# Kernel optimization log

Hardware: AMD Instinct MI355X
Metric: run time of the kernel (lower is better)

## Reference

```python
import jax, jax.numpy as jnp
import numpy as np

N = 100000
E = 1600000
F_IN = 256   # 4 * 64 after concat
H = 128

def _glorot(key, shape):
    fan_in, fan_out = shape
    lim = jnp.sqrt(6.0 / (fan_in + fan_out))
    return jax.random.uniform(key, shape, jnp.float32, -lim, lim)

def setup_inputs() -> dict:
    key = jax.random.key(0)
    ks = jax.random.split(key, 32)
    inp = {
        'x': jax.random.normal(ks[0], (N, 64), jnp.float32),
        'diff': jax.random.normal(ks[1], (N, 64), jnp.float32),
        'rec_prev': jax.random.normal(ks[2], (N, 64), jnp.float32),
        'hidden_prev': jax.random.normal(ks[3], (N, 64), jnp.float32),
        'edge_index': jax.random.randint(ks[4], (2, E), 0, N, jnp.int64),
    }
    dims = [(F_IN, H), (H, H), (H, H), (H, 1)]
    for i, (din, dout) in enumerate(dims):
        inp[f'Wl{i}'] = _glorot(ks[5 + 3 * i], (din, dout))  # neighbor (aggr) weight
        inp[f'Wr{i}'] = _glorot(ks[6 + 3 * i], (din, dout))  # root weight
        inp[f'b{i}'] = jnp.zeros((dout,), jnp.float32)
    return inp

def _sage_conv(h, src, dst, Wl, Wr, b):
    # mean aggregation of source-node features at destination nodes (PyG SAGEConv)
    msg_sum = jax.ops.segment_sum(h[src], dst, num_segments=N)        # [N, F]
    cnt = jax.ops.segment_sum(jnp.ones((src.shape[0],), h.dtype), dst, num_segments=N)
    mean = msg_sum / jnp.maximum(cnt, 1.0)[:, None]
    return mean @ Wl + h @ Wr + b

def reference(x, diff, rec_prev, hidden_prev, edge_index,
              Wl0, Wr0, b0, Wl1, Wr1, b1, Wl2, Wr2, b2, Wl3, Wr3, b3):
    src, dst = edge_index[0], edge_index[1]
    h = jnp.concatenate([x, diff, rec_prev, hidden_prev], axis=1)  # [N, 256]
    params = [(Wl0, Wr0, b0), (Wl1, Wr1, b1), (Wl2, Wr2, b2), (Wl3, Wr3, b3)]
    h = _sage_conv(h, src, dst, *params[0])
    for Wl, Wr, b in params[1:]:
        h = jax.nn.relu(h)
        h = _sage_conv(h, src, dst, Wl, Wr, b)
    out = jax.nn.sigmoid(h)          # [N, 1]
    lwp_util = jnp.mean(out)
    return out, lwp_util
```

## Files before the change

### kernel.cpp

```cpp
#include <hip/hip_runtime.h>
#include <hip/hip_bf16.h>

#define NN 100000
#define EE 1600000
#define HH 128
#define NB 391
#define CAP 5120
#define GB 1563

typedef short bf16x8 __attribute__((ext_vector_type(8)));
typedef short bf16x4 __attribute__((ext_vector_type(4)));
typedef float f32x4  __attribute__((ext_vector_type(4)));

__device__ inline short f2bf(float v) {
    __hip_bfloat16 b = __float2bfloat16(v);
    return *reinterpret_cast<short*>(&b);
}

typedef __attribute__((address_space(1))) void gvoid_t;
typedef __attribute__((address_space(3))) void svoid_t;
__device__ __forceinline__ void gload16(const void* g, void* l) {
    __builtin_amdgcn_global_load_lds((gvoid_t*)g, (svoid_t*)l, 16, 0, 0);
}

__device__ __forceinline__ void waitbar(int n) {
    if (n == 0)      asm volatile("s_waitcnt vmcnt(0)\n\ts_barrier" ::: "memory");
    else if (n == 2) asm volatile("s_waitcnt vmcnt(2)\n\ts_barrier" ::: "memory");
    else             asm volatile("s_waitcnt vmcnt(4)\n\ts_barrier" ::: "memory");
}

__global__ __launch_bounds__(1024) void prep_kernel(
    const float* __restrict__ Wl0, const float* __restrict__ Wr0,
    const float* __restrict__ Wl1, const float* __restrict__ Wr1,
    const float* __restrict__ Wl2, const float* __restrict__ Wr2,
    __hip_bfloat16* __restrict__ WT0, __hip_bfloat16* __restrict__ WT1,
    __hip_bfloat16* __restrict__ WT2, int* __restrict__ bcur) {
    const int t = threadIdx.x;
    if (blockIdx.x == 128) {
        if (t < NB) bcur[t] = 0;
        return;
    }
    int id = blockIdx.x * 1024 + t;
    if (id < 65536) {
        int k = id & 255, n = id >> 8;
        float v = (n < 128) ? Wl0[(size_t)k * 128 + n]
                            : Wr0[(size_t)k * 128 + (n - 128)];
        WT0[(size_t)n * 256 + k] = __float2bfloat16(v);
    } else {
        id -= 65536;
        int layer = id >> 15;
        int u = id & 32767;
        int k = u & 127, n = u >> 7;
        const float* Wl = layer ? Wl2 : Wl1;
        const float* Wr = layer ? Wr2 : Wr1;
        __hip_bfloat16* WT = layer ? WT2 : WT1;
        float v = (n < 128) ? Wl[(size_t)k * 128 + n]
                            : Wr[(size_t)k * 128 + (n - 128)];
        WT[(size_t)n * 128 + k] = __float2bfloat16(v);
    }
}

#define TSW 152
template <int K, bool FIRST>
__device__ __forceinline__ void gemm_body(
    short* __restrict__ lsh, int bid,
    const __hip_bfloat16* hin,
    const float* __restrict__ x0, const float* __restrict__ x1,
    const float* __restrict__ x2, const float* __restrict__ x3,
    const __hip_bfloat16* __restrict__ wt, const float* __restrict__ bias,
    __hip_bfloat16* zout, __hip_bfloat16* __restrict__ rout) {
    const int t    = threadIdx.x;
    const int w    = t >> 6;
    const int lane = t & 63;
    const int quad = lane >> 4;
    const int l16  = lane & 15;
    const int n0   = bid * 64;

    constexpr int NS   = K / 64;
    constexpr int BUFB = FIRST ? 16384 : 8192;
    constexpr int GPW  = FIRST ? 4 : 2;
    char* const lc = (char*)lsh;

    const __hip_bfloat16* afeat[4];
#pragma unroll
    for (int ft = 0; ft < 4; ++ft)
        afeat[ft] = wt + (size_t)(w * 64 + ft * 16 + l16) * K + quad * 8;

    f32x4 acc[4][4];
#pragma unroll
    for (int ft = 0; ft < 4; ++ft)
#pragma unroll
        for (int nt = 0; nt < 4; ++nt)
            acc[ft][nt] = (f32x4){0.f, 0.f, 0.f, 0.f};

    auto stage = [&](int p, int bb) {
        char* lb = lc + bb * BUFB;
        if constexpr (FIRST) {
            const float* sp = (p == 0) ? x0 : (p == 1) ? x1 : (p == 2) ? x2 : x3;
#pragma unroll
            for (int i = 0; i < 4; ++i) {
                const int j   = w * 4 + i;
                const int row = j * 4 + (lane >> 4);
                int rg = n0 + row; if (rg > NN - 1) rg = NN - 1;
                const int colb = ((lane & 15) * 16) ^ ((row & 15) << 4);
                gload16((const char*)sp + (size_t)rg * 256 + colb, lb + j * 1024);
            }
        } else {
#pragma unroll
            for (int i = 0; i < 2; ++i) {
                const int j   = w * 2 + i;
                const int row = j * 8 + (lane >> 3);
                int rg = n0 + row; if (rg > NN - 1) rg = NN - 1;
                const int colb = ((lane & 7) * 16) ^ ((row & 7) << 4);
                gload16((const char*)hin + (size_t)rg * 256 + p * 128 + colb,
                        lb + j * 1024);
            }
        }
    };

    auto compute = [&](int s) {
        const char* lb = lc + (s & 1) * BUFB;
#pragma unroll
        for (int kcl = 0; kcl < 2; ++kcl) {
            const int kc = s * 2 + kcl;
            bf16x8 af[4];
#pragma unroll
            for (int ft = 0; ft < 4; ++ft)
                af[ft] = *(const bf16x8*)(afeat[ft] + kc * 32);
#pragma unroll
            for (int nt = 0; nt < 4; ++nt) {
                const int row = nt * 16 + l16;
                bf16x8 b;
                if constexpr (FIRST) {
                    const int sw = (row & 15) << 4;
                    const int B0 = kcl * 128 + quad * 32;
                    const char* rb = lb + row * 256;
                    const f32x4 lo = *(const f32x4*)(rb + ((B0) ^ sw));
                    const f32x4 hi = *(const f32x4*)(rb + ((B0 + 16) ^ sw));
                    b[0] = f2bf(lo[0]); b[1] = f2bf(lo[1]);
                    b[2] = f2bf(lo[2]); b[3] = f2bf(lo[3]);
                    b[4] = f2bf(hi[0]); b[5] = f2bf(hi[1]);
                    b[6] = f2bf(hi[2]); b[7] = f2bf(hi[3]);
                } else {
                    const int sw = (row & 7) << 4;
                    const int B0 = kcl * 64 + quad * 16;
                    b = *(const bf16x8*)(lb + row * 128 + (B0 ^ sw));
                }
#pragma unroll
                for (int ft = 0; ft < 4; ++ft)
                    acc[ft][nt] = __builtin_amdgcn_mfma_f32_16x16x32_bf16(
                        af[ft], b, acc[ft][nt], 0, 0, 0);
            }
        }
    };

    stage(0, 0);
    stage(1, 1);
#pragma unroll
    for (int s = 0; s < NS; ++s) {
        waitbar(s < NS - 1 ? GPW : 0);
        compute(s);
        asm volatile("s_barrier" ::: "memory");
        if (s + 2 < NS) stage(s + 2, s & 1);
    }

    if (w < 2) {
#pragma unroll
        for (int ft = 0; ft < 4; ++ft) {
            const int fb = ft * 16 + quad * 4;
#pragma unroll
            for (int nt = 0; nt < 4; ++nt) {
                const f32x4 a = acc[ft][nt];
                bf16x4 p;
                p[0] = f2bf(a[0]); p[1] = f2bf(a[1]);
                p[2] = f2bf(a[2]); p[3] = f2bf(a[3]);
                *(bf16x4*)&lsh[(nt * 16 + l16) * TSW + w * 64 + fb] = p;
            }
        }
    }
    __syncthreads();
#pragma unroll
    for (int u = 0; u < 4; ++u) {
        const int id  = u * 256 + t;
        const int row = id >> 4, ch = (id & 15) * 8;
        const int nd  = n0 + row;
        if (nd < NN)
            *(bf16x8*)&zout[(size_t)nd * HH + ch] = *(const bf16x8*)&lsh[row * TSW + ch];
    }
    __syncthreads();

    if (w >= 2) {
        const int fcol = (w - 2) * 64;
#pragma unroll
        for (int ft = 0; ft < 4; ++ft) {
            const int fb = ft * 16 + quad * 4;
            const float4 bv = *(const float4*)&bias[fcol + fb];
#pragma unroll
            for (int nt = 0; nt < 4; ++nt) {
                const f32x4 a = acc[ft][nt];
                bf16x4 p;
                p[0] = f2bf(a[0] + bv.x); p[1] = f2bf(a[1] + bv.y);
                p[2] = f2bf(a[2] + bv.z); p[3] = f2bf(a[3] + bv.w);
                *(bf16x4*)&lsh[(nt * 16 + l16) * TSW + fcol + fb] = p;
            }
        }
    }
    __syncthreads();
#pragma unroll
    for (int u = 0; u < 4; ++u) {
        const int id  = u * 256 + t;
        const int row = id >> 4, ch = (id & 15) * 8;
        const int nd  = n0 + row;
        if (nd < NN)
            *(bf16x8*)&rout[(size_t)nd * HH + ch] = *(const bf16x8*)&lsh[row * TSW + ch];
    }
}

template <int K, bool FIRST>
__global__ __launch_bounds__(256) void gemm_kernel(
    const __hip_bfloat16* hin,
    const float* __restrict__ x0, const float* __restrict__ x1,
    const float* __restrict__ x2, const float* __restrict__ x3,
    const __hip_bfloat16* __restrict__ wt, const float* __restrict__ bias,
    __hip_bfloat16* zout, __hip_bfloat16* __restrict__ rout) {
    __shared__ short lsh[9728];
    gemm_body<K, FIRST>(lsh, blockIdx.x, hin, x0, x1, x2, x3, wt, bias, zout, rout);
}

__global__ __launch_bounds__(256) void gemm0_scatter_kernel(
    const float* __restrict__ x0, const float* __restrict__ x1,
    const float* __restrict__ x2, const float* __restrict__ x3,
    const __hip_bfloat16* __restrict__ wt, const float* __restrict__ bias,
    __hip_bfloat16* __restrict__ zout, __hip_bfloat16* __restrict__ rout,
    const int* __restrict__ srcv, const int* __restrict__ dstv,
    int* __restrict__ bcur, int* __restrict__ pairs) {
    __shared__ short lsh[16384];
    const int t = threadIdx.x;

    if (blockIdx.x >= NB) {
        gemm_body<256, true>(lsh, blockIdx.x - NB, nullptr, x0, x1, x2, x3,
                             wt, bias, zout, rout);
        return;
    }

    int* hist = (int*)lsh;
    int* base = hist + NB;
    for (int j = t; j < NB; j += 256) hist[j] = 0;
    __syncthreads();

    const int e0 = blockIdx.x * 4096;
    int s[16], d[16];
#pragma unroll
    for (int u = 0; u < 16; ++u) {
        const int e = e0 + u * 256 + t;
        if (e < EE) {
            s[u] = srcv[e]; d[u] = dstv[e];
            atomicAdd(&hist[d[u] >> 8], 1);
        } else {
            d[u] = -1;
        }
    }
    __syncthreads();

    for (int j = t; j < NB; j += 256)
        base[j] = hist[j] ? atomicAdd(&bcur[j], hist[j]) : 0;
    __syncthreads();
    for (int j = t; j < NB; j += 256) hist[j] = base[j];
    __syncthreads();

#pragma unroll
    for (int u = 0; u < 16; ++u)
        if (d[u] >= 0) {
            const int b   = d[u] >> 8;
            const int pos = atomicAdd(&hist[b], 1);
            if (pos < CAP) pairs[b * CAP + pos] = (s[u] << 8) | (d[u] & 255);
        }
}

__global__ __launch_bounds__(256) void finalize_kernel(
    const int* __restrict__ bcur, const int* __restrict__ pairs,
    int* __restrict__ csr, int* __restrict__ beg, int* __restrict__ eend,
    float* __restrict__ inv) {
    __shared__ int cnt[256];
    __shared__ int scn[256];
    __shared__ int cur[256];
    const int b = blockIdx.x, t = threadIdx.x;
    int m = bcur[b];
    if (m > CAP) m = CAP;

    cnt[t] = 0;
    __syncthreads();
    for (int e = t; e < m; e += 256)
        atomicAdd(&cnt[pairs[b * CAP + e] & 255], 1);
    __syncthreads();

    const int v = cnt[t];
    scn[t] = v;
    __syncthreads();
    for (int st = 1; st < 256; st <<= 1) {
        int tv = (t >= st) ? scn[t - st] : 0;
        __syncthreads();
        scn[t] += tv;
        __syncthreads();
    }
    const int myStart = scn[t] - v;
    cur[t] = myStart;
    __syncthreads();

    for (int e = t; e < m; e += 256) {
        const int pk  = pairs[b * CAP + e];
        const int pos = atomicAdd(&cur[pk & 255], 1);
        csr[b * CAP + pos] = pk >> 8;
    }

    const int node = b * 256 + t;
    if (node < NN) {
        beg[node]  = b * CAP + myStart;
        eend[node] = b * CAP + myStart + v;
        inv[node]  = 1.0f / fmaxf((float)v, 1.0f);
    }
}

template <bool LAST>
__global__ __launch_bounds__(256) void aggregate_kernel(
    const __hip_bfloat16* __restrict__ z, __hip_bfloat16* __restrict__ rio,
    const int* __restrict__ beg, const int* __restrict__ eend,
    const int* __restrict__ csr, const float* __restrict__ inv,
    const float* __restrict__ Wl3, const float* __restrict__ Wr3,
    const float* __restrict__ b3, float* __restrict__ z3,
    float* __restrict__ r3) {
    const int i    = (blockIdx.x * 256 + threadIdx.x) >> 6;
    const int lane = threadIdx.x & 63;
    const int g    = lane >> 4;
    const int l16  = lane & 15;
    if (i >= NN) return;
    const int b0 = beg[i], e0 = eend[i];

    float acc[8];
#pragma unroll
    for (int j = 0; j < 8; ++j) acc[j] = 0.f;

    int e = b0 + g;
    for (; e + 12 < e0; e += 16) {
        const int s0 = csr[e];
        const int s1 = csr[e + 4];
        const int s2 = csr[e + 8];
        const int s3 = csr[e + 12];
        const bf16x8 z0 = *(const bf16x8*)&z[(size_t)s0 * HH + l16 * 8];
        const bf16x8 z1 = *(const bf16x8*)&z[(size_t)s1 * HH + l16 * 8];
        const bf16x8 z2 = *(const bf16x8*)&z[(size_t)s2 * HH + l16 * 8];
        const bf16x8 z3v = *(const bf16x8*)&z[(size_t)s3 * HH + l16 * 8];
        const __hip_bfloat162* p0 = (const __hip_bfloat162*)&z0;
        const __hip_bfloat162* p1 = (const __hip_bfloat162*)&z1;
        const __hip_bfloat162* p2 = (const __hip_bfloat162*)&z2;
        const __hip_bfloat162* p3 = (const __hip_bfloat162*)&z3v;
#pragma unroll
        for (int j = 0; j < 4; ++j) {
            acc[2 * j]     += __bfloat162float(p0[j].x) + __bfloat162float(p1[j].x)
                            + __bfloat162float(p2[j].x) + __bfloat162float(p3[j].x);
            acc[2 * j + 1] += __bfloat162float(p0[j].y) + __bfloat162float(p1[j].y)
                            + __bfloat162float(p2[j].y) + __bfloat162float(p3[j].y);
        }
    }
    for (; e < e0; e += 4) {
        const int s0 = csr[e];
        const bf16x8 z0 = *(const bf16x8*)&z[(size_t)s0 * HH + l16 * 8];
        const __hip_bfloat162* p0 = (const __hip_bfloat162*)&z0;
#pragma unroll
        for (int j = 0; j < 4; ++j) {
            acc[2 * j]     += __bfloat162float(p0[j].x);
            acc[2 * j + 1] += __bfloat162float(p0[j].y);
        }
    }

#pragma unroll
    for (int j = 0; j < 8; ++j) {
        acc[j] += __shfl_xor(acc[j], 16, 64);
        acc[j] += __shfl_xor(acc[j], 32, 64);
    }

    const float iv = inv[i];
    const int   f  = l16 * 8 + g * 2;
    const __hip_bfloat162 rv = *(const __hip_bfloat162*)&rio[(size_t)i * HH + f];
    const float ox = fmaxf(acc[g * 2]     * iv + __bfloat162float(rv.x), 0.f);
    const float oy = fmaxf(acc[g * 2 + 1] * iv + __bfloat162float(rv.y), 0.f);

    if (!LAST) {
        __hip_bfloat162 o;
        o.x = __float2bfloat16(ox);
        o.y = __float2bfloat16(oy);
        *(__hip_bfloat162*)&rio[(size_t)i * HH + f] = o;
    } else {
        const float2 wl = *(const float2*)&Wl3[f];
        const float2 wr = *(const float2*)&Wr3[f];
        float al = ox * wl.x + oy * wl.y;
        float ar = ox * wr.x + oy * wr.y;
#pragma unroll
        for (int m = 32; m; m >>= 1) {
            al += __shfl_xor(al, m, 64);
            ar += __shfl_xor(ar, m, 64);
        }
        if (lane == 0) {
            z3[i] = al;
            r3[i] = ar + b3[0];
        }
    }
}

__global__ __launch_bounds__(256) void final_kernel(
    const float* __restrict__ z3, const float* __restrict__ r3,
    const int* __restrict__ beg, const int* __restrict__ eend,
    const int* __restrict__ csr, const float* __restrict__ inv,
    float* __restrict__ out, float* __restrict__ partial) {
    __shared__ float red[4];
    const int i    = (blockIdx.x * 256 + threadIdx.x) >> 6;
    const int lane = threadIdx.x & 63;
    const int w    = threadIdx.x >> 6;
    float v = 0.f;
    if (i < NN) {
        const int b0 = beg[i], e0 = eend[i];
        float a = 0.f;
        for (int e = b0 + lane; e < e0; e += 64) a += z3[csr[e]];
#pragma unroll
        for (int m = 32; m; m >>= 1) a += __shfl_xor(a, m, 64);
        const float pre = a * inv[i] + r3[i];
        const float s = 1.f / (1.f + __expf(-pre));
        if (lane == 0) { out[i] = s; v = s; }
    }
    if (lane == 0) red[w] = v;
    __syncthreads();
    if (threadIdx.x == 0)
        partial[blockIdx.x] = red[0] + red[1] + red[2] + red[3];
}

__global__ __launch_bounds__(256) void mean_kernel(const float* __restrict__ partial,
                                                   int nb, float* __restrict__ out) {
    __shared__ float lds[256];
    float s = 0.f;
    for (int i = threadIdx.x; i < nb; i += 256) s += partial[i];
    lds[threadIdx.x] = s;
    __syncthreads();
    for (int st = 128; st; st >>= 1) {
        if (threadIdx.x < st) lds[threadIdx.x] += lds[threadIdx.x + st];
        __syncthreads();
    }
    if (threadIdx.x == 0) out[NN] = lds[0] / (float)NN;
}

extern "C" void kernel_launch(void* const* d_in, const int* in_sizes, int n_in,
                              void* d_out, int out_size, void* d_ws, size_t ws_size,
                              hipStream_t stream) {
    const float* x    = (const float*)d_in[0];
    const float* diff = (const float*)d_in[1];
    const float* rec  = (const float*)d_in[2];
    const float* hid  = (const float*)d_in[3];
    const int* edge   = (const int*)d_in[4];
    const int* esrc = edge;
    const int* edst = edge + EE;
    const float* Wl0 = (const float*)d_in[5];
    const float* Wr0 = (const float*)d_in[6];
    const float* b0  = (const float*)d_in[7];
    const float* Wl1 = (const float*)d_in[8];
    const float* Wr1 = (const float*)d_in[9];
    const float* b1  = (const float*)d_in[10];
    const float* Wl2 = (const float*)d_in[11];
    const float* Wr2 = (const float*)d_in[12];
    const float* b2  = (const float*)d_in[13];
    const float* Wl3 = (const float*)d_in[14];
    const float* Wr3 = (const float*)d_in[15];
    const float* b3  = (const float*)d_in[16];
    float* out = (float*)d_out;

    char* w = (char*)d_ws;
    auto alloc = [&](size_t bytes) -> void* {
        void* p = (void*)w;
        w += (bytes + 255) & ~(size_t)255;
        return p;
    };
    __hip_bfloat16* bufA = (__hip_bfloat16*)alloc((size_t)NN * HH * 2);
    __hip_bfloat16* bufB = (__hip_bfloat16*)alloc((size_t)NN * HH * 2);
    __hip_bfloat16* WT0  = (__hip_bfloat16*)alloc((size_t)256 * 256 * 2);
    __hip_bfloat16* WT1  = (__hip_bfloat16*)alloc((size_t)256 * 128 * 2);
    __hip_bfloat16* WT2  = (__hip_bfloat16*)alloc((size_t)256 * 128 * 2);
    int*   pairs   = (int*)alloc((size_t)NB * CAP * 4);
    int*   csr     = (int*)alloc((size_t)NB * CAP * 4);
    int*   bcur    = (int*)alloc((size_t)512 * 4);
    int*   beg     = (int*)alloc((size_t)NN * 4);
    int*   eend    = (int*)alloc((size_t)NN * 4);
    float* inv     = (float*)alloc((size_t)NN * 4);
    float* z3      = (float*)alloc((size_t)NN * 4);
    float* r3      = (float*)alloc((size_t)NN * 4);
    float* partial = (float*)alloc((size_t)25000 * 4);

    const int WB = (NN + 3) / 4;

    prep_kernel<<<129, 1024, 0, stream>>>(Wl0, Wr0, Wl1, Wr1, Wl2, Wr2,
                                          WT0, WT1, WT2, bcur);

    gemm0_scatter_kernel<<<GB + NB, 256, 0, stream>>>(
        x, diff, rec, hid, WT0, b0, bufA, bufB, esrc, edst, bcur, pairs);

    finalize_kernel<<<NB, 256, 0, stream>>>(bcur, pairs, csr, beg, eend, inv);

    aggregate_kernel<false><<<WB, 256, 0, stream>>>(bufA, bufB, beg, eend, csr, inv,
                                                    nullptr, nullptr, nullptr,
                                                    nullptr, nullptr);

    gemm_kernel<128, false><<<GB, 256, 0, stream>>>(bufB, nullptr, nullptr, nullptr, nullptr,
                                                    WT1, b1, bufB, bufA);
    aggregate_kernel<false><<<WB, 256, 0, stream>>>(bufB, bufA, beg, eend, csr, inv,
                                                    nullptr, nullptr, nullptr,
                                                    nullptr, nullptr);

    gemm_kernel<128, false><<<GB, 256, 0, stream>>>(bufA, nullptr, nullptr, nullptr, nullptr,
                                                    WT2, b2, bufA, bufB);
    aggregate_kernel<true><<<WB, 256, 0, stream>>>(bufA, bufB, beg, eend, csr, inv,
                                                   Wl3, Wr3, b3, z3, r3);

    final_kernel<<<WB, 256, 0, stream>>>(z3, r3, beg, eend, csr, inv, out, partial);
    mean_kernel<<<1, 256, 0, stream>>>(partial, WB, out);
}
```

Before: 500.0 us.

## Prefetch weight fragments into registers, triple-buffer layer-0 staging, merge epilogue

The GEMM body now loads the weight A-fragments into a double-buffered register array ahead of use instead of inside the compute step. The main loop is replaced by a hand-scheduled sequence with explicit vmcnt waits. Layer 0 uses three LDS buffers so two input stages stay in flight. The two-pass epilogue (z then root+bias, each with its own syncs) becomes a single pass writing both halves into a wider LDS tile. This cuts barriers and global traffic, in exchange for more LDS per block (lower occupancy possible) and brittle vmcnt counts tied to the exact load ordering.

Measured after the change: 499.1 us. No clear change (-0.2%).

```diff
diff --git a/kernel.cpp b/kernel.cpp
--- a/kernel.cpp
+++ b/kernel.cpp
@@ -23,10 +23,28 @@
     __builtin_amdgcn_global_load_lds((gvoid_t*)g, (svoid_t*)l, 16, 0, 0);
 }
 
-__device__ __forceinline__ void waitbar(int n) {
-    if (n == 0)      asm volatile("s_waitcnt vmcnt(0)\n\ts_barrier" ::: "memory");
-    else if (n == 2) asm volatile("s_waitcnt vmcnt(2)\n\ts_barrier" ::: "memory");
-    else             asm volatile("s_waitcnt vmcnt(4)\n\ts_barrier" ::: "memory");
+__device__ __forceinline__ void ld_fence() { asm volatile("" ::: "memory"); }
+
+template <int N>
+__device__ __forceinline__ void wait_vm_bar() {
+    if constexpr (N == 0)
+        asm volatile("s_waitcnt vmcnt(0)\n\ts_barrier" ::: "memory");
+    else if constexpr (N == 8)
+        asm volatile("s_waitcnt vmcnt(8)\n\ts_barrier" ::: "memory");
+    else if constexpr (N == 12)
+        asm volatile("s_waitcnt vmcnt(12)\n\ts_barrier" ::: "memory");
+    else if constexpr (N == 16)
+        asm volatile("s_waitcnt vmcnt(16)\n\ts_barrier" ::: "memory");
+    else if constexpr (N == 18)
+        asm volatile("s_waitcnt vmcnt(18)\n\ts_barrier" ::: "memory");
+    else if constexpr (N == 20)
+        asm volatile("s_waitcnt vmcnt(20)\n\ts_barrier" ::: "memory");
+    else
+        static_assert(N == 0 || N == 8 || N == 12 || N == 16 || N == 18 || N == 20,
+                      "bad N");
+}
+__device__ __forceinline__ void barrier_only() {
+    asm volatile("s_barrier" ::: "memory");
 }
 
 __global__ __launch_bounds__(1024) void prep_kernel(
@@ -60,7 +78,7 @@
     }
 }
 
-#define TSW 152
+#define EW 264
 template <int K, bool FIRST>
 __device__ __forceinline__ void gemm_body(
     short* __restrict__ lsh, int bid,
@@ -76,9 +94,7 @@
     const int l16  = lane & 15;
     const int n0   = bid * 64;
 
-    constexpr int NS   = K / 64;
     constexpr int BUFB = FIRST ? 16384 : 8192;
-    constexpr int GPW  = FIRST ? 4 : 2;
     char* const lc = (char*)lsh;
 
     const __hip_bfloat16* afeat[4];
@@ -92,6 +108,17 @@
 #pragma unroll
         for (int nt = 0; nt < 4; ++nt)
             acc[ft][nt] = (f32x4){0.f, 0.f, 0.f, 0.f};
+
+    bf16x8 wreg[2][8];
+
+    auto loadW = [&](int p, int pb) {
+#pragma unroll
+        for (int kcl = 0; kcl < 2; ++kcl)
+#pragma unroll
+            for (int ft = 0; ft < 4; ++ft)
+                wreg[pb][kcl * 4 + ft] =
+                    *(const bf16x8*)(afeat[ft] + (p * 2 + kcl) * 32);
+    };
 
     auto stage = [&](int p, int bb) {
         char* lb = lc + bb * BUFB;
@@ -118,15 +145,10 @@
         }
     };
 
-    auto compute = [&](int s) {
-        const char* lb = lc + (s & 1) * BUFB;
+    auto compute = [&](int s, int bb, int pb) {
+        const char* lb = lc + bb * BUFB;
 #pragma unroll
         for (int kcl = 0; kcl < 2; ++kcl) {
-            const int kc = s * 2 + kcl;
-            bf16x8 af[4];
-#pragma unroll
-            for (int ft = 0; ft < 4; ++ft)
-                af[ft] = *(const bf16x8*)(afeat[ft] + kc * 32);
 #pragma unroll
             for (int nt = 0; nt < 4; ++nt) {
                 const int row = nt * 16 + l16;
@@ -149,70 +171,53 @@
 #pragma unroll
                 for (int ft = 0; ft < 4; ++ft)
                     acc[ft][nt] = __builtin_amdgcn_mfma_f32_16x16x32_bf16(
-                        af[ft], b, acc[ft][nt], 0, 0, 0);
+                        wreg[pb][kcl * 4 + ft], b, acc[ft][nt], 0, 0, 0);
             }
         }
     };
 
-    stage(0, 0);
-    stage(1, 1);
-#pragma unroll
-    for (int s = 0; s < NS; ++s) {
-        waitbar(s < NS - 1 ? GPW : 0);
-        compute(s);
-        asm volatile("s_barrier" ::: "memory");
-        if (s + 2 < NS) stage(s + 2, s & 1);
-    }
-
-    if (w < 2) {
-#pragma unroll
-        for (int ft = 0; ft < 4; ++ft) {
-            const int fb = ft * 16 + quad * 4;
-#pragma unroll
-            for (int nt = 0; nt < 4; ++nt) {
-                const f32x4 a = acc[ft][nt];
-                bf16x4 p;
-                p[0] = f2bf(a[0]); p[1] = f2bf(a[1]);
-                p[2] = f2bf(a[2]); p[3] = f2bf(a[3]);
-                *(bf16x4*)&lsh[(nt * 16 + l16) * TSW + w * 64 + fb] = p;
-            }
-        }
-    }
-    __syncthreads();
-#pragma unroll
-    for (int u = 0; u < 4; ++u) {
+    if constexpr (FIRST) {
+        stage(0, 0); ld_fence();
+        stage(1, 1); ld_fence();
+        loadW(0, 0); ld_fence();
+        wait_vm_bar<12>(); loadW(1, 1); stage(2, 2); compute(0, 0, 0); barrier_only();
+        wait_vm_bar<20>(); loadW(2, 0); stage(3, 0); compute(1, 1, 1); barrier_only();
+        wait_vm_bar<12>(); loadW(3, 1);              compute(2, 2, 0); barrier_only();
+        wait_vm_bar<8>();                            compute(3, 0, 1); barrier_only();
+    } else {
+        stage(0, 0); ld_fence();
+        stage(1, 1); ld_fence();
+        loadW(0, 0); loadW(1, 1);
+        wait_vm_bar<18>(); compute(0, 0, 0); barrier_only();
+        wait_vm_bar<16>(); compute(1, 1, 1); barrier_only();
+    }
+
+#pragma unroll
+    for (int ft = 0; ft < 4; ++ft) {
+        const int fb = ft * 16 + quad * 4;
+        float4 bv = make_float4(0.f, 0.f, 0.f, 0.f);
+        if (w >= 2) bv = *(const float4*)&bias[(w - 2) * 64 + fb];
+        const int cbase = (w & 1) * 64 + ((w >= 2) ? 128 : 0);
+#pragma unroll
+        for (int nt = 0; nt < 4; ++nt) {
+            const f32x4 a = acc[ft][nt];
+            bf16x4 p;
+            p[0] = f2bf(a[0] + bv.x); p[1] = f2bf(a[1] + bv.y);
+            p[2] = f2bf(a[2] + bv.z); p[3] = f2bf(a[3] + bv.w);
+            *(bf16x4*)&lsh[(nt * 16 + l16) * EW + cbase + fb] = p;
+        }
+    }
+    __syncthreads();
+#pragma unroll
+    for (int u = 0; u < 8; ++u) {
         const int id  = u * 256 + t;
-        const int row = id >> 4, ch = (id & 15) * 8;
+        const int row = id >> 5, ch = (id & 31) * 8;
         const int nd  = n0 + row;
-        if (nd < NN)
-            *(bf16x8*)&zout[(size_t)nd * HH + ch] = *(const bf16x8*)&lsh[row * TSW + ch];
-    }
-    __syncthreads();
-
-    if (w >= 2) {
-        const int fcol = (w - 2) * 64;
-#pragma unroll
-        for (int ft = 0; ft < 4; ++ft) {
-            const int fb = ft * 16 + quad * 4;
-            const float4 bv = *(const float4*)&bias[fcol + fb];
-#pragma unroll
-            for (int nt = 0; nt < 4; ++nt) {
-                const f32x4 a = acc[ft][nt];
-                bf16x4 p;
-                p[0] = f2bf(a[0] + bv.x); p[1] = f2bf(a[1] + bv.y);
-                p[2] = f2bf(a[2] + bv.z); p[3] = f2bf(a[3] + bv.w);
-                *(bf16x4*)&lsh[(nt * 16 + l16) * TSW + fcol + fb] = p;
-            }
-        }
-    }
-    __syncthreads();
-#pragma unroll
-    for (int u = 0; u < 4; ++u) {
-        const int id  = u * 256 + t;
-        const int row = id >> 4, ch = (id & 15) * 8;
-        const int nd  = n0 + row;
-        if (nd < NN)
-            *(bf16x8*)&rout[(size_t)nd * HH + ch] = *(const bf16x8*)&lsh[row * TSW + ch];
+        if (nd < NN) {
+            const bf16x8 v = *(const bf16x8*)&lsh[row * EW + ch];
+            if (ch < 128) *(bf16x8*)&zout[(size_t)nd * HH + ch] = v;
+            else          *(bf16x8*)&rout[(size_t)nd * HH + (ch - 128)] = v;
+        }
     }
 }
 
@@ -223,7 +228,7 @@
     const float* __restrict__ x2, const float* __restrict__ x3,
     const __hip_bfloat16* __restrict__ wt, const float* __restrict__ bias,
     __hip_bfloat16* zout, __hip_bfloat16* __restrict__ rout) {
-    __shared__ short lsh[9728];
+    __shared__ short lsh[16896];
     gemm_body<K, FIRST>(lsh, blockIdx.x, hin, x0, x1, x2, x3, wt, bias, zout, rout);
 }
 
@@ -234,7 +239,7 @@
     __hip_bfloat16* __restrict__ zout, __hip_bfloat16* __restrict__ rout,
     const int* __restrict__ srcv, const int* __restrict__ dstv,
     int* __restrict__ bcur, int* __restrict__ pairs) {
-    __shared__ short lsh[16384];
+    __shared__ short lsh[24576];
     const int t = threadIdx.x;
 
     if (blockIdx.x >= NB) {
```
